# Performance work log

Hardware: AMD Instinct MI355X
Metric: run time of the kernel (lower is better)

Reference implementation:

```python
import jax, jax.numpy as jnp
import numpy as np

P, K, D = 512, 4, 256          # identities, instances per id per modality, feature dim
N = 2 * P * K                  # two modality halves, as assumed by mod_idxs in the module
R_STRENGTH = 2.0               # cmrr_loss __init__ r=2.0 (soft_rank regularization_strength)


def _soft_rank_kl(values, reg_strength):
    """torchsort.soft_rank(values, regularization='kl', strength=reg_strength), rows of length n.

    theta = values/strength; sort descending -> s; w = [n,...,1].
    isotonic_kl solves argmin_{v noninc} <e^{s-v},1> + <w, v>; block value on [i..j] is
    LSE(s[i:j+1]) - LSE(log w[i:j+1]). Min-max formula (valid for PAV-solvable problems):
      dual_k = min_{i<=k} max_{j>=k} B[i,j].
    ranks = exp(s - dual) scattered back by the inverse permutation.
    """
    n = values.shape[1]
    theta = values * (1.0 / reg_strength)
    perm = jnp.argsort(-theta, axis=1)                     # descending sort order
    s = jnp.take_along_axis(theta, perm, axis=1)
    inv_perm = jnp.argsort(perm, axis=1)
    logw = jnp.log(jnp.arange(n, 0, -1, dtype=values.dtype))  # log([n, n-1, ..., 1])
    k = jnp.arange(n)
    ii, jj, kk = k[:, None, None], k[None, :, None], k[None, None, :]
    # segment [i, max(i,j)]; for invalid i>j it degenerates to {i} so LSE stays finite (no NaN grads)
    seg = (kk >= ii) & (kk <= jnp.maximum(jj, ii))         # (n, n, n) indexed [i, j, k]
    neg = jnp.asarray(-jnp.inf, values.dtype)
    lse_s = jax.nn.logsumexp(jnp.where(seg[None], s[:, None, None, :], neg), axis=-1)  # (R,n,n)
    lse_w = jax.nn.logsumexp(jnp.where(seg, logw[None, None, :], neg), axis=-1)        # (n,n)
    valid = k[:, None] <= k[None, :]                       # i <= j
    B = jnp.where(valid[None], lse_s - lse_w[None], neg)   # block values, -inf where invalid
    T = jax.lax.cummax(B, axis=2, reverse=True)            # T[:,i,k] = max_{j>=k} B[:,i,j]
    tri = k[:, None] <= k[None, :]                         # i <= k
    dual = jnp.min(jnp.where(tri[None], T, jnp.inf), axis=1)  # (R, n), nonincreasing
    return jnp.exp(jnp.take_along_axis(s - dual, inv_perm, axis=1))


def _pairwise_dist(f):
    # ||f_i - f_j||_2 with clamp(min=1e-12) before sqrt, as in the module
    sq = jnp.sum(f * f, axis=1)
    d2 = sq[:, None] + sq[None, :] - 2.0 * (f @ f.T)
    return jnp.sqrt(jnp.clip(d2, 1e-12, None))


def _spearman(a, b):
    a = a - jnp.mean(a, axis=1, keepdims=True)
    a = a / jnp.linalg.norm(a, axis=1, keepdims=True)
    b = b - jnp.mean(b, axis=1, keepdims=True)
    b = b / jnp.linalg.norm(b, axis=1, keepdims=True)
    return jnp.sum(a * b, axis=1)


def setup_inputs() -> dict:
    key = jax.random.key(0)
    k0, k1, k2 = jax.random.split(key, 3)
    ids = jnp.repeat(jnp.arange(P), K)                     # PK sampling within each modality
    target = jnp.concatenate([ids, ids])                   # first half modality 0, second half modality 1
    f0 = jax.random.normal(k0, (N, D), jnp.float32)
    f1 = jax.random.normal(k1, (N, D), jnp.float32)
    f2 = jax.random.normal(k2, (N, D), jnp.float32)
    return {"f0": f0, "f1": f1, "f2": f2, "target": target, "k_pos": K}


def reference(f0, f1, f2, target, k_pos):
    feats = (f0, f1, f2)
    n = target.shape[0]
    pos = target[None, :] == target[:, None]
    mod = jnp.concatenate([jnp.zeros(n // 2, jnp.int32), jnp.ones(n // 2, jnp.int32)])
    mask = pos & (mod[None, :] != mod[:, None])            # pos_idxs & ~mod_idxs
    # boolean-mask gather dists[mask].view(N,-1): per row, the k_pos True columns in increasing order
    idx = jnp.argsort(jnp.where(mask, 0, 1), axis=1, stable=True)[:, :k_pos]
    ranks = []
    for f in feats:
        dists = _pairwise_dist(f)
        dist_intra = jnp.take_along_axis(dists, idx, axis=1)   # (N, k_pos)
        ranks.append(_soft_rank_kl(dist_intra, R_STRENGTH))
    L = len(feats)
    loss = jnp.zeros((n,), f0.dtype)
    for i in range(L):
        for j in range(i + 1, L):
            loss = loss + (_spearman(ranks[i], ranks[j]) + 1.0) / 2.0
    loss = loss / (L * (L - 1) / 2.0)
    return jnp.mean(loss)
```

## Files before the change

### kernel.cpp

```cpp
#include <hip/hip_runtime.h>
#include <hip/hip_bf16.h>


__device__ __forceinline__ void soft_rank4(const float d2[4], float r[4]) {
    float th[4]; int p[4] = {0, 1, 2, 3};
#pragma unroll
    for (int t = 0; t < 4; ++t) th[t] = 0.5f * sqrtf(fmaxf(d2[t], 1e-12f));
#define CSWAP(a, b)                                                           \
    if (th[a] < th[b]) {                                                      \
        float tt = th[a]; th[a] = th[b]; th[b] = tt;                          \
        int tp = p[a]; p[a] = p[b]; p[b] = tp;                                \
    }
    CSWAP(0, 1) CSWAP(1, 2) CSWAP(2, 3) CSWAP(0, 1) CSWAP(1, 2) CSWAP(0, 1)
#undef CSWAP
    const float logW[4][4] = {
        {1.3862944f, 1.9459101f, 2.1972246f, 2.3025851f},
        {0.f,        1.0986123f, 1.6094379f, 1.7917595f},
        {0.f,        0.f,        0.6931472f, 1.0986123f},
        {0.f,        0.f,        0.f,        0.f}};
    float B[4][4];
#pragma unroll
    for (int i = 0; i < 4; ++i) {
        float run = 0.f;
#pragma unroll
        for (int j = 0; j < 4; ++j) {
            if (j >= i) {
                run += __expf(th[j] - th[i]);
                B[i][j] = th[i] + __logf(run) - logW[i][j];
            }
        }
    }
    float rs[4];
#pragma unroll
    for (int k = 0; k < 4; ++k) {
        float dual = 1e30f;
#pragma unroll
        for (int i = 0; i < 4; ++i) {
            if (i <= k) {
                float mx = -1e30f;
#pragma unroll
                for (int j = 0; j < 4; ++j)
                    if (j >= k) mx = fmaxf(mx, B[i][j]);
                dual = fminf(dual, mx);
            }
        }
        rs[k] = __expf(th[k] - dual);
    }
#pragma unroll
    for (int t = 0; t < 4; ++t) {
        float v = rs[3];
        v = (p[2] == t) ? rs[2] : v;
        v = (p[1] == t) ? rs[1] : v;
        v = (p[0] == t) ? rs[0] : v;
        r[t] = v;
    }
}

__device__ __forceinline__ float spearman4(const float a[4], const float b[4]) {
    float ma = 0.25f * (a[0] + a[1] + a[2] + a[3]);
    float mb = 0.25f * (b[0] + b[1] + b[2] + b[3]);
    float sab = 0.f, saa = 0.f, sbb = 0.f;
#pragma unroll
    for (int t = 0; t < 4; ++t) {
        float x = a[t] - ma, y = b[t] - mb;
        sab += x * y; saa += x * x; sbb += y * y;
    }
    return sab * rsqrtf(saa * sbb);
}

__device__ __forceinline__ float row_loss(const float d2a[3][4]) {
    float ranks[3][4];
#pragma unroll
    for (int f = 0; f < 3; ++f) soft_rank4(d2a[f], ranks[f]);
    const float c01 = spearman4(ranks[0], ranks[1]);
    const float c02 = spearman4(ranks[0], ranks[2]);
    const float c12 = spearman4(ranks[1], ranks[2]);
    return (c01 + c02 + c12 + 3.f) * (0.5f / 3.f);
}

__global__ __launch_bounds__(64) void cmrr_main(
        const float* __restrict__ f0, const float* __restrict__ f1,
        const float* __restrict__ f2, const int* __restrict__ target,
        float* __restrict__ partials, int N) {
    const float* F[3] = {f0, f1, f2};
    const int g = blockIdx.x;
    const int lane = threadIdx.x;
    const int half = N >> 1;
    const int id = target[4 * g];
    const int jbase = half + 4 * id;

    float4 A[3][4], Bv[3][4];
#pragma unroll
    for (int f = 0; f < 3; ++f) {
        const float4* pa = (const float4*)(F[f] + (size_t)(4 * g) * 256);
#pragma unroll
        for (int i = 0; i < 4; ++i) A[f][i] = pa[i * 64 + lane];
    }
#pragma unroll
    for (int f = 0; f < 3; ++f) {
        const float4* pb = (const float4*)(F[f] + (size_t)jbase * 256);
#pragma unroll
        for (int j = 0; j < 4; ++j) Bv[f][j] = pb[j * 64 + lane];
    }

    float c[64];
#pragma unroll
    for (int f = 0; f < 3; ++f) {
#pragma unroll
        for (int i = 0; i < 4; ++i) {
#pragma unroll
            for (int j = 0; j < 4; ++j) {
                const float4 a = A[f][i], b = Bv[f][j];
                const float dx = a.x - b.x, dy = a.y - b.y;
                const float dz = a.z - b.z, dw = a.w - b.w;
                c[f * 16 + i * 4 + j] = dx * dx + dy * dy + dz * dz + dw * dw;
            }
        }
    }
#pragma unroll
    for (int v = 48; v < 64; ++v) c[v] = 0.f;

#pragma unroll
    for (int s = 0; s < 6; ++s) {
        const int bit = 1 << s;
        const bool hi = (lane & bit) != 0;
#pragma unroll
        for (int k = 0; k < 32; ++k) {
            if (k < (32 >> s)) {
                const float lo_v = c[2 * k], hi_v = c[2 * k + 1];
                const float send = hi ? lo_v : hi_v;
                const float recv = __shfl_xor(send, bit, 64);
                c[k] = (hi ? hi_v : lo_v) + recv;
            }
        }
    }
    const float red = c[0];

    const int r = lane & 7;
    const bool isRow = r < 4;
    float d2[3][4];
#pragma unroll
    for (int f = 0; f < 3; ++f) {
#pragma unroll
        for (int t = 0; t < 4; ++t) {
            const int src = f * 16 + (isRow ? (r * 4 + t) : (t * 4 + (r - 4)));
            d2[f][t] = __shfl(red, src, 64);
        }
    }
    float loss = row_loss(d2);
    loss = (lane < 8) ? loss : 0.f;
#pragma unroll
    for (int m = 32; m >= 1; m >>= 1) loss += __shfl_xor(loss, m, 64);

    if (lane == 0) partials[g] = loss;
}

__global__ __launch_bounds__(64) void cmrr_reduce(
        const float* __restrict__ partials, float* __restrict__ out,
        int nparts, float inv_n) {
    float s = 0.f;
    for (int i = threadIdx.x; i < nparts; i += 64) s += partials[i];
#pragma unroll
    for (int m = 32; m >= 1; m >>= 1) s += __shfl_xor(s, m, 64);
    if (threadIdx.x == 0) out[0] = s * inv_n;
}

extern "C" void kernel_launch(void* const* d_in, const int* in_sizes, int n_in,
                              void* d_out, int out_size, void* d_ws,
                              size_t ws_size, hipStream_t stream) {
    const float* f0 = (const float*)d_in[0];
    const float* f1 = (const float*)d_in[1];
    const float* f2 = (const float*)d_in[2];
    const int* target = (const int*)d_in[3];
    const int N = in_sizes[3];
    const int ngroups = N / 8;
    float* parts = (float*)d_ws;
    cmrr_main<<<ngroups, 64, 0, stream>>>(f0, f1, f2, target, parts, N);
    cmrr_reduce<<<1, 64, 0, stream>>>(parts, (float*)d_out, ngroups,
                                      1.0f / (float)N);
}
```

Baseline: 74.87 us.

## Replace second reduce kernel with fixed-point atomic last-block reduction

Drops the separate single-block reduce kernel. Each block now quantizes its partial loss to a fixed-point integer and adds it to a 64-bit accumulator with one atomic, which also increments a block counter packed in the high bits. The block that sees the final count writes the mean. This saves a kernel launch but adds a memset launch and rounds each partial to fixed point, which costs a little precision and assumes partials are non-negative and the sum fits in 52 bits.

```diff
diff --git a/kernel.cpp b/kernel.cpp
--- a/kernel.cpp
+++ b/kernel.cpp
@@ -1,6 +1,7 @@
 #include <hip/hip_runtime.h>
-#include <hip/hip_bf16.h>
 
+
+#define FXP_SCALE 67108864.0f
 
 __device__ __forceinline__ void soft_rank4(const float d2[4], float r[4]) {
     float th[4]; int p[4] = {0, 1, 2, 3};
@@ -81,7 +82,7 @@
 __global__ __launch_bounds__(64) void cmrr_main(
         const float* __restrict__ f0, const float* __restrict__ f1,
         const float* __restrict__ f2, const int* __restrict__ target,
-        float* __restrict__ partials, int N) {
+        unsigned long long* __restrict__ acc, float* __restrict__ out, int N) {
     const float* F[3] = {f0, f1, f2};
     const int g = blockIdx.x;
     const int lane = threadIdx.x;
@@ -152,17 +153,16 @@
 #pragma unroll
     for (int m = 32; m >= 1; m >>= 1) loss += __shfl_xor(loss, m, 64);
 
-    if (lane == 0) partials[g] = loss;
-}
-
-__global__ __launch_bounds__(64) void cmrr_reduce(
-        const float* __restrict__ partials, float* __restrict__ out,
-        int nparts, float inv_n) {
-    float s = 0.f;
-    for (int i = threadIdx.x; i < nparts; i += 64) s += partials[i];
-#pragma unroll
-    for (int m = 32; m >= 1; m >>= 1) s += __shfl_xor(s, m, 64);
-    if (threadIdx.x == 0) out[0] = s * inv_n;
+    if (lane == 0) {
+        const unsigned long long q =
+            (unsigned long long)(loss * FXP_SCALE + 0.5f);
+        const unsigned long long pkt = (1ULL << 52) | q;
+        const unsigned long long old = atomicAdd(acc, pkt);
+        if ((old >> 52) == (unsigned long long)(gridDim.x - 1)) {
+            const unsigned long long total = (old + q) & ((1ULL << 52) - 1ULL);
+            out[0] = (float)((double)total / (double)FXP_SCALE / (double)N);
+        }
+    }
 }
 
 extern "C" void kernel_launch(void* const* d_in, const int* in_sizes, int n_in,
@@ -174,8 +174,9 @@
     const int* target = (const int*)d_in[3];
     const int N = in_sizes[3];
     const int ngroups = N / 8;
-    float* parts = (float*)d_ws;
-    cmrr_main<<<ngroups, 64, 0, stream>>>(f0, f1, f2, target, parts, N);
-    cmrr_reduce<<<1, 64, 0, stream>>>(parts, (float*)d_out, ngroups,
-                                      1.0f / (float)N);
+    unsigned long long* acc = (unsigned long long*)d_ws;
+
+    hipMemsetAsync(acc, 0, sizeof(unsigned long long), stream);
+    cmrr_main<<<ngroups, 64, 0, stream>>>(f0, f1, f2, target, acc,
+                                          (float*)d_out, N);
 }
```

Result: slower. 78.11 us (+4.3%).
